# Optimization experiments

Measured on AMD Instinct MI355X. Metric: run time of the kernel, lower is better.

## Reference

```python
import jax, jax.numpy as jnp
import numpy as np

# Sizes: irreps = 16x0e + 8x1o, sh = 1x0e + 1x1o (l_max=1)
N = 50000          # nodes
E = 400000         # edges
MUL0 = 16          # scalar (0e) multiplicity == hidden_dim
MUL1 = 8           # vector (1o) multiplicity
DIM = MUL0 + 3 * MUL1   # 40
RMLP = 64
# FullyConnectedTensorProduct paths (uvw):
#  P1: 0e x 0e -> 0e  w:(16,16)   P2: 1o x 1o -> 0e  w:(8,16)
#  P3: 0e x 1o -> 1o  w:(16,8)    P4: 1o x 0e -> 1o  w:(8,8)
WNUM = MUL0*MUL0 + MUL1*MUL0 + MUL0*MUL1 + MUL1*MUL1  # 576
# e3nn normalization (irrep_normalization='component', path_normalization='element'):
#  out 0e: alpha = 1 / (16*1 + 8*1);  out 1o: alpha = 3 / (16*1 + 8*1)
N0 = float(np.sqrt(1.0 / 24.0))
N1 = float(np.sqrt(3.0 / 24.0))
INV_SQRT3 = float(1.0 / np.sqrt(3.0))  # wigner-3j entries for (1,1,0),(0,1,1),(1,0,1)


def setup_inputs() -> dict:
    key = jax.random.key(0)
    ks = jax.random.split(key, 8)
    h = jax.random.normal(ks[0], (N, DIM), jnp.float32)
    edge_index = jax.random.randint(ks[1], (2, E), 0, N)
    edge_vec = jax.random.normal(ks[2], (E, 3), jnp.float32)
    edge_len = jax.random.uniform(ks[3], (E,), jnp.float32)
    mlp_w1 = jax.random.normal(ks[4], (1, RMLP), jnp.float32)
    mlp_b1 = jnp.zeros((RMLP,), jnp.float32)
    mlp_w2 = jax.random.normal(ks[5], (RMLP, WNUM), jnp.float32) / np.sqrt(RMLP)
    mlp_b2 = jnp.zeros((WNUM,), jnp.float32)
    gate_w = jax.random.normal(ks[6], (MUL0, 3 * MUL1), jnp.float32) / np.sqrt(MUL0)
    gate_b = jnp.zeros((3 * MUL1,), jnp.float32)
    return dict(h=h, edge_index=edge_index, edge_vec=edge_vec, edge_len=edge_len,
                mlp_w1=mlp_w1, mlp_b1=mlp_b1, mlp_w2=mlp_w2, mlp_b2=mlp_b2,
                gate_w=gate_w, gate_b=gate_b)


def reference(h, edge_index, edge_vec, edge_len,
              mlp_w1, mlp_b1, mlp_w2, mlp_b2, gate_w, gate_b):
    sender, receiver = edge_index[0], edge_index[1]
    n = h.shape[0]

    # spherical harmonics, normalize=True, normalization='component'
    # l=0 -> 1.0 ; l=1 -> sqrt(3) * unit(edge_vec)
    unit = edge_vec / jnp.linalg.norm(edge_vec, axis=-1, keepdims=True)
    sh1 = jnp.sqrt(jnp.float32(3.0)) * unit                      # (E,3)

    # radial MLP -> per-edge tensor-product weights
    w = jax.nn.silu(edge_len[:, None] @ mlp_w1 + mlp_b1) @ mlp_w2 + mlp_b2  # (E,576)
    o1 = MUL0 * MUL0; o2 = o1 + MUL1 * MUL0; o3 = o2 + MUL0 * MUL1
    W1 = w[:, :o1].reshape(-1, MUL0, MUL0)
    W2 = w[:, o1:o2].reshape(-1, MUL1, MUL0)
    W3 = w[:, o2:o3].reshape(-1, MUL0, MUL1)
    W4 = w[:, o3:].reshape(-1, MUL1, MUL1)

    # gather sender features and split into scalars / vectors
    hg = h[sender]                                                # (E,40)
    hs = hg[:, :MUL0]                                             # (E,16)
    hv = hg[:, MUL0:].reshape(-1, MUL1, 3)                        # (E,8,3)

    # tensor product (per-edge weighted CG contraction)
    dot = jnp.einsum('euk,ek->eu', hv, sh1)                       # 1o.1o -> 0e
    out_s = N0 * (jnp.einsum('eu,euw->ew', hs, W1)
                  + INV_SQRT3 * jnp.einsum('eu,euw->ew', dot, W2))  # (E,16)
    t3 = jnp.einsum('eu,euw->ew', hs, W3)                         # (E,8)
    t4 = jnp.einsum('euk,euw->ewk', hv, W4)                       # (E,8,3)
    out_v = (N1 * INV_SQRT3) * (t3[:, :, None] * sh1[:, None, :] + t4)

    msg = jnp.concatenate([out_s, out_v.reshape(-1, 3 * MUL1)], axis=-1)  # (E,40)

    # scatter-add into nodes
    agg = jax.ops.segment_sum(msg, receiver, num_segments=n)      # (N,40)

    # scalar gating of non-scalar channels + residual
    gate = jax.nn.sigmoid(h[:, :MUL0] @ gate_w + gate_b)          # (N,24)
    agg = jnp.concatenate([agg[:, :MUL0], agg[:, MUL0:] * gate], axis=-1)
    return h + agg
```

## Files before the change

### kernel.cpp

```cpp
#include <hip/hip_runtime.h>
#include <hip/hip_fp16.h>

typedef _Float16 half8  __attribute__((ext_vector_type(8)));
typedef _Float16 half2v __attribute__((ext_vector_type(2)));
typedef float    float4v __attribute__((ext_vector_type(4)));

namespace {
constexpr int N_NODES = 50000;
constexpr int N_EDGES = 400000;
constexpr int MUL0 = 16;
constexpr int MUL1 = 8;
constexpr int DIM  = 40;
constexpr int RMLP = 64;
constexpr int WNUM = 576;
constexpr int GE   = 256;
constexpr int NGROUP = (N_EDGES + GE - 1) / GE;
constexpr int GRID = 256;
constexpr int WST = 80, AST = 80, FST = 56;
constexpr int OFF_ACT  = 92160;
constexpr int OFF_FEAT = 133120;
constexpr int OFF_RCV  = 161792;
constexpr int LDS_BYTES = 162816;
constexpr float C_N0 = 0.2041241452319315f;
constexpr float C_NV = 0.3535533905932738f * 0.5773502691896258f;
constexpr float C_INV3 = 0.5773502691896258f;
constexpr float C_SQRT3 = 1.7320508075688772f;
}

#define MFMA16(a, b, c) __builtin_amdgcn_mfma_f32_16x16x32_f16((a), (b), (c), 0, 0, 0)

__device__ inline void h2_atomic_add(__half2* addr, __half2 val) {
#if __has_builtin(__builtin_amdgcn_flat_atomic_fadd_v2f16)
    half2v v = *reinterpret_cast<half2v*>(&val);
    (void)__builtin_amdgcn_flat_atomic_fadd_v2f16(
        reinterpret_cast<half2v*>(addr), v);
#else
    unsigned int* ai = reinterpret_cast<unsigned int*>(addr);
    unsigned int old = *ai, assumed;
    do {
        assumed = old;
        __half2 cur = *reinterpret_cast<__half2*>(&assumed);
        __half2 sum = __hadd2(cur, val);
        unsigned int nv = *reinterpret_cast<unsigned int*>(&sum);
        old = atomicCAS(ai, assumed, nv);
    } while (old != assumed);
#endif
}

__global__ __launch_bounds__(512, 1) void edge_fused3(
    const float* __restrict__ h,
    const int*   __restrict__ ei,
    const float* __restrict__ evec,
    const float* __restrict__ elen,
    const float* __restrict__ w1,
    const float* __restrict__ b1,
    const float* __restrict__ w2,
    const float* __restrict__ b2,
    __half2*     __restrict__ agg2)
{
    extern __shared__ char smem[];
    _Float16* w2L  = (_Float16*)smem;
    _Float16* actL = (_Float16*)(smem + OFF_ACT);
    _Float16* featL= (_Float16*)(smem + OFF_FEAT);
    int*      rcvL = (int*)(smem + OFF_RCV);

    const int t = threadIdx.x;

    for (int i = t; i < RMLP * WNUM; i += 512) {
        const int r = i / WNUM;
        const int j = i - r * WNUM;
        w2L[j * WST + r] = (_Float16)w2[i];
    }

    const int lane = t & 63, wid = t >> 6;
    const int l15 = lane & 15, lg = lane >> 4;
    const int usel = lg >> 1;

    __half2 pOS[2][2];
    __half2 pV[2][6];
    int pR[2] = {0, 0};
    int pValid[2] = {0, 0};
    bool havePrev = false;

    for (int g = blockIdx.x; g < NGROUP; g += GRID) {
        if (havePrev) {
#pragma unroll
            for (int tt = 0; tt < 2; ++tt) {
                if (pValid[tt]) {
                    __half2* a2 = agg2 + (long)pR[tt] * 20;
                    h2_atomic_add(a2 + lg * 2 + 0, pOS[tt][0]);
                    h2_atomic_add(a2 + lg * 2 + 1, pOS[tt][1]);
                    if (lg < 2) {
#pragma unroll
                        for (int r2 = 0; r2 < 6; ++r2)
                            h2_atomic_add(a2 + 8 + 6 * lg + r2, pV[tt][r2]);
                    }
                }
            }
        }

        const int base = g * GE;
        const int cnt = (N_EDGES - base < GE) ? (N_EDGES - base) : GE;

        {
            const int el = t >> 1, q = t & 1;
            _Float16* fr = featL + el * FST;
            if (el < cnt) {
                const int eg = base + el;
                const int snd = ei[eg];
                const float* hp = h + (long)snd * DIM;
#pragma unroll
                for (int i = 0; i < 20; ++i)
                    fr[q * 20 + i] = (_Float16)hp[q * 20 + i];
                if (q == 0) {
                    rcvL[el] = ei[N_EDGES + eg];
                    const float v0 = evec[3 * eg + 0];
                    const float v1 = evec[3 * eg + 1];
                    const float v2 = evec[3 * eg + 2];
                    const float rinv = rsqrtf(v0 * v0 + v1 * v1 + v2 * v2) * C_SQRT3;
                    fr[40] = (_Float16)(v0 * rinv);
                    fr[41] = (_Float16)(v1 * rinv);
                    fr[42] = (_Float16)(v2 * rinv);
                }
                const float len = elen[eg];
#pragma unroll
                for (int i = 0; i < 4; ++i) {
                    half8 av;
#pragma unroll
                    for (int j2 = 0; j2 < 8; ++j2) {
                        const int r = q * 32 + i * 8 + j2;
                        const float tv = fmaf(len, w1[r], b1[r]);
                        av[j2] = (_Float16)(tv / (1.0f + __expf(-tv)));
                    }
                    *(half8*)&actL[el * AST + q * 32 + i * 8] = av;
                }
            } else {
                const half8 z = {};
#pragma unroll
                for (int i = 0; i < 20; ++i) fr[q * 20 + i] = (_Float16)0.f;
                if (q == 0) {
                    rcvL[el] = 0;
                    fr[40] = fr[41] = fr[42] = (_Float16)0.f;
                }
#pragma unroll
                for (int i = 0; i < 4; ++i)
                    *(half8*)&actL[el * AST + q * 32 + i * 8] = z;
            }
        }
        __syncthreads();

        {
            const int el = t >> 1;
            const int ub = (t & 1) * 4;
            const _Float16* fr = featL + el * FST;
            const float s0 = (float)fr[40], s1 = (float)fr[41], s2 = (float)fr[42];
#pragma unroll
            for (int j2 = 0; j2 < 4; ++j2) {
                const int u = ub + j2;
                const float d = (float)fr[16 + 3 * u + 0] * s0
                              + (float)fr[16 + 3 * u + 1] * s1
                              + (float)fr[16 + 3 * u + 2] * s2;
                featL[el * FST + 44 + u] = (_Float16)(C_INV3 * d);
            }
        }
        __syncthreads();

        {
            const int et0 = wid * 2;
            half8 B[2][2];
#pragma unroll
            for (int tt = 0; tt < 2; ++tt)
#pragma unroll
                for (int s = 0; s < 2; ++s)
                    B[tt][s] = *(const half8*)&actL[((et0 + tt) * 16 + l15) * AST + s * 32 + lg * 8];

            const float4v zz = {0.f, 0.f, 0.f, 0.f};
            float4v os0 = zz, os1 = zz;
            float4v t30 = zz, t31 = zz;
            float4v t4a0 = zz, t4a1 = zz, t4a2 = zz;
            float4v t4b0 = zz, t4b1 = zz, t4b2 = zz;

            const _Float16* fA = featL + ((et0 + 0) * 16 + l15) * FST;
            const _Float16* fB = featL + ((et0 + 1) * 16 + l15) * FST;

#pragma unroll
            for (int jp = 0; jp < 8; ++jp) {
                const half2v hA = *(const half2v*)&fA[2 * jp];
                const half2v hB = *(const half2v*)&fB[2 * jp];
#pragma unroll
                for (int h2 = 0; h2 < 2; ++h2) {
                    const int jt = 2 * jp + h2;
                    const float4v binit = *(const float4v*)&b2[jt * 16 + lg * 4];
                    const _Float16* wr = &w2L[(jt * 16 + l15) * WST];
                    const half8 w0 = *(const half8*)&wr[lg * 8];
                    const half8 w1v = *(const half8*)&wr[32 + lg * 8];
                    float4v d0 = MFMA16(w0, B[0][0], binit); d0 = MFMA16(w1v, B[0][1], d0);
                    float4v d1 = MFMA16(w0, B[1][0], binit); d1 = MFMA16(w1v, B[1][1], d1);
                    os0 += (float)hA[h2] * d0;
                    os1 += (float)hB[h2] * d1;
                }
            }
#pragma unroll
            for (int jp = 0; jp < 4; ++jp) {
                const half2v hA = *(const half2v*)&fA[44 + 2 * jp];
                const half2v hB = *(const half2v*)&fB[44 + 2 * jp];
#pragma unroll
                for (int h2 = 0; h2 < 2; ++h2) {
                    const int jt = 16 + 2 * jp + h2;
                    const float4v binit = *(const float4v*)&b2[jt * 16 + lg * 4];
                    const _Float16* wr = &w2L[(jt * 16 + l15) * WST];
                    const half8 w0 = *(const half8*)&wr[lg * 8];
                    const half8 w1v = *(const half8*)&wr[32 + lg * 8];
                    float4v d0 = MFMA16(w0, B[0][0], binit); d0 = MFMA16(w1v, B[0][1], d0);
                    float4v d1 = MFMA16(w0, B[1][0], binit); d1 = MFMA16(w1v, B[1][1], d1);
                    os0 += (float)hA[h2] * d0;
                    os1 += (float)hB[h2] * d1;
                }
            }
#pragma unroll
            for (int jt = 24; jt < 32; ++jt) {
                const int u = 2 * (jt - 24) + usel;
                const float4v binit = *(const float4v*)&b2[jt * 16 + lg * 4];
                const _Float16* wr = &w2L[(jt * 16 + l15) * WST];
                const half8 w0 = *(const half8*)&wr[lg * 8];
                const half8 w1v = *(const half8*)&wr[32 + lg * 8];
                float4v d0 = MFMA16(w0, B[0][0], binit); d0 = MFMA16(w1v, B[0][1], d0);
                float4v d1 = MFMA16(w0, B[1][0], binit); d1 = MFMA16(w1v, B[1][1], d1);
                t30 += (float)fA[u] * d0;
                t31 += (float)fB[u] * d1;
            }
#pragma unroll
            for (int jt = 32; jt < 36; ++jt) {
                const int u = 2 * (jt - 32) + usel;
                const float4v binit = *(const float4v*)&b2[jt * 16 + lg * 4];
                const _Float16* wr = &w2L[(jt * 16 + l15) * WST];
                const half8 w0 = *(const half8*)&wr[lg * 8];
                const half8 w1v = *(const half8*)&wr[32 + lg * 8];
                float4v d0 = MFMA16(w0, B[0][0], binit); d0 = MFMA16(w1v, B[0][1], d0);
                float4v d1 = MFMA16(w0, B[1][0], binit); d1 = MFMA16(w1v, B[1][1], d1);
                t4a0 += (float)fA[16 + 3 * u + 0] * d0;
                t4a1 += (float)fA[16 + 3 * u + 1] * d0;
                t4a2 += (float)fA[16 + 3 * u + 2] * d0;
                t4b0 += (float)fB[16 + 3 * u + 0] * d1;
                t4b1 += (float)fB[16 + 3 * u + 1] * d1;
                t4b2 += (float)fB[16 + 3 * u + 2] * d1;
            }

#pragma unroll
            for (int r = 0; r < 4; ++r) {
                t30[r] += __shfl_xor(t30[r], 32);
                t31[r] += __shfl_xor(t31[r], 32);
                t4a0[r] += __shfl_xor(t4a0[r], 32);
                t4a1[r] += __shfl_xor(t4a1[r], 32);
                t4a2[r] += __shfl_xor(t4a2[r], 32);
                t4b0[r] += __shfl_xor(t4b0[r], 32);
                t4b1[r] += __shfl_xor(t4b1[r], 32);
                t4b2[r] += __shfl_xor(t4b2[r], 32);
            }

#pragma unroll
            for (int tt = 0; tt < 2; ++tt) {
                const int el = (et0 + tt) * 16 + l15;
                pValid[tt] = (el < cnt);
                pR[tt] = rcvL[el];
                const float4v& os = tt ? os1 : os0;
                pOS[tt][0] = __floats2half2_rn(C_N0 * os[0], C_N0 * os[1]);
                pOS[tt][1] = __floats2half2_rn(C_N0 * os[2], C_N0 * os[3]);
                const _Float16* fr = featL + el * FST;
                const float s0 = (float)fr[40], s1 = (float)fr[41], s2 = (float)fr[42];
                const float4v& t3 = tt ? t31 : t30;
                const float4v& x0 = tt ? t4b0 : t4a0;
                const float4v& x1 = tt ? t4b1 : t4a1;
                const float4v& x2 = tt ? t4b2 : t4a2;
                float vv[12];
#pragma unroll
                for (int r = 0; r < 4; ++r) {
                    vv[3 * r + 0] = C_NV * (x0[r] + t3[r] * s0);
                    vv[3 * r + 1] = C_NV * (x1[r] + t3[r] * s1);
                    vv[3 * r + 2] = C_NV * (x2[r] + t3[r] * s2);
                }
#pragma unroll
                for (int r2 = 0; r2 < 6; ++r2)
                    pV[tt][r2] = __floats2half2_rn(vv[2 * r2], vv[2 * r2 + 1]);
            }
        }
        __syncthreads();
        havePrev = true;
    }

    if (havePrev) {
#pragma unroll
        for (int tt = 0; tt < 2; ++tt) {
            if (pValid[tt]) {
                __half2* a2 = agg2 + (long)pR[tt] * 20;
                h2_atomic_add(a2 + lg * 2 + 0, pOS[tt][0]);
                h2_atomic_add(a2 + lg * 2 + 1, pOS[tt][1]);
                if (lg < 2) {
#pragma unroll
                    for (int r2 = 0; r2 < 6; ++r2)
                        h2_atomic_add(a2 + 8 + 6 * lg + r2, pV[tt][r2]);
                }
            }
        }
    }
}

__global__ __launch_bounds__(256) void node_kernel2(
    const float* __restrict__ h,
    const float* __restrict__ gw,
    const float* __restrict__ gb,
    const __half2* __restrict__ agg2,
    float*       __restrict__ out)
{
    const int n = blockIdx.x * 256 + threadIdx.x;
    if (n >= N_NODES) return;
    const float* hp = h + (long)n * DIM;
    float* op = out + (long)n * DIM;
    const __half2* ar = agg2 + (long)n * 20;

    float ag[DIM];
#pragma unroll
    for (int i = 0; i < 20; ++i) {
        const float2 f = __half22float2(ar[i]);
        ag[2 * i] = f.x;
        ag[2 * i + 1] = f.y;
    }

    float hsv[MUL0];
#pragma unroll
    for (int u = 0; u < MUL0; ++u) hsv[u] = hp[u];
#pragma unroll
    for (int i = 0; i < MUL0; ++i) op[i] = hsv[i] + ag[i];

#pragma unroll 1
    for (int j = 0; j < 3 * MUL1; ++j) {
        float a = gb[j];
#pragma unroll
        for (int u = 0; u < MUL0; ++u) a = fmaf(hsv[u], gw[u * (3 * MUL1) + j], a);
        const float g = 1.0f / (1.0f + __expf(-a));
        op[MUL0 + j] = fmaf(ag[MUL0 + j], g, hp[MUL0 + j]);
    }
}

extern "C" void kernel_launch(void* const* d_in, const int* in_sizes, int n_in,
                              void* d_out, int out_size, void* d_ws, size_t ws_size,
                              hipStream_t stream)
{
    const float* h    = (const float*)d_in[0];
    const int*   ei   = (const int*)d_in[1];
    const float* evec = (const float*)d_in[2];
    const float* elen = (const float*)d_in[3];
    const float* w1   = (const float*)d_in[4];
    const float* b1   = (const float*)d_in[5];
    const float* w2   = (const float*)d_in[6];
    const float* b2   = (const float*)d_in[7];
    const float* gw   = (const float*)d_in[8];
    const float* gb   = (const float*)d_in[9];
    float* out = (float*)d_out;
    __half2* agg2 = (__half2*)d_ws;

    (void)hipFuncSetAttribute((const void*)edge_fused3,
                              hipFuncAttributeMaxDynamicSharedMemorySize,
                              LDS_BYTES);

    (void)hipMemsetAsync(d_ws, 0, (size_t)N_NODES * DIM * sizeof(__half), stream);
    edge_fused3<<<GRID, 512, LDS_BYTES, stream>>>(
        h, ei, evec, elen, w1, b1, w2, b2, agg2);
    node_kernel2<<<(N_NODES + 255) / 256, 256, 0, stream>>>(h, gw, gb, agg2, out);
}
```

Baseline: 359.2 us.

## Replace atomic scatter with CSR sort and per-node gather of edge messages

Builds a receiver-sorted CSR permutation each call (histogram, single-block scan, fill) and has the edge kernel write per-edge fp16 messages to a buffer, not atomically adding into node accumulators. A new node kernel gathers each node's messages through the permutation, sums them in fp32, and applies gating and the residual. This removes the fp16 packed atomics and the accumulator memset, at the cost of three extra launches, a serial scan over 50k nodes in one block, and writing and re-reading a 32 MB message buffer. The new path runs only if the workspace is large enough; otherwise the old path is kept.

```diff
diff --git a/kernel.cpp b/kernel.cpp
--- a/kernel.cpp
+++ b/kernel.cpp
@@ -2,6 +2,7 @@
 #include <hip/hip_fp16.h>
 
 typedef _Float16 half8  __attribute__((ext_vector_type(8)));
+typedef _Float16 half4s __attribute__((ext_vector_type(4)));
 typedef _Float16 half2v __attribute__((ext_vector_type(2)));
 typedef float    float4v __attribute__((ext_vector_type(4)));
 
@@ -21,6 +22,12 @@
 constexpr int OFF_FEAT = 133120;
 constexpr int OFF_RCV  = 161792;
 constexpr int LDS_BYTES = 162816;
+constexpr size_t MSG_OFF    = 0;
+constexpr size_t PERM_OFF   = 32000000;
+constexpr size_t ROWPTR_OFF = 33600000;
+constexpr size_t CNT_OFF    = 33800064;
+constexpr size_t CUR_OFF    = 34000064;
+constexpr size_t CSR_REQ    = 34200064;
 constexpr float C_N0 = 0.2041241452319315f;
 constexpr float C_NV = 0.3535533905932738f * 0.5773502691896258f;
 constexpr float C_INV3 = 0.5773502691896258f;
@@ -47,6 +54,326 @@
 #endif
 }
 
+__global__ __launch_bounds__(256) void hist_k(const int* __restrict__ ei,
+                                              int* __restrict__ cnt) {
+    const int e = blockIdx.x * 256 + threadIdx.x;
+    if (e < N_EDGES) atomicAdd(&cnt[ei[N_EDGES + e]], 1);
+}
+
+__global__ __launch_bounds__(1024) void scan_k(const int* __restrict__ cnt,
+                                               int* __restrict__ rowptr) {
+    __shared__ int s[1024];
+    const int t = threadIdx.x;
+    constexpr int CH = 49;
+    const int b0 = t * CH;
+    int sum = 0;
+    for (int i = 0; i < CH; ++i) {
+        const int idx = b0 + i;
+        if (idx < N_NODES) sum += cnt[idx];
+    }
+    s[t] = sum;
+    __syncthreads();
+    for (int o = 1; o < 1024; o <<= 1) {
+        const int x = (t >= o) ? s[t - o] : 0;
+        __syncthreads();
+        s[t] += x;
+        __syncthreads();
+    }
+    int run = s[t] - sum;
+    for (int i = 0; i < CH; ++i) {
+        const int idx = b0 + i;
+        if (idx < N_NODES) { rowptr[idx] = run; run += cnt[idx]; }
+    }
+    if (t == 0) rowptr[N_NODES] = N_EDGES;
+}
+
+__global__ __launch_bounds__(256) void fill_k(const int* __restrict__ ei,
+                                              const int* __restrict__ rowptr,
+                                              int* __restrict__ cursor,
+                                              int* __restrict__ perm) {
+    const int e = blockIdx.x * 256 + threadIdx.x;
+    if (e < N_EDGES) {
+        const int r = ei[N_EDGES + e];
+        const int pos = rowptr[r] + atomicAdd(&cursor[r], 1);
+        perm[pos] = e;
+    }
+}
+
+__global__ __launch_bounds__(512, 1) void edge_msg(
+    const float* __restrict__ h,
+    const int*   __restrict__ ei,
+    const float* __restrict__ evec,
+    const float* __restrict__ elen,
+    const float* __restrict__ w1,
+    const float* __restrict__ b1,
+    const float* __restrict__ w2,
+    const float* __restrict__ b2,
+    _Float16*    __restrict__ msg)
+{
+    extern __shared__ char smem[];
+    _Float16* w2L  = (_Float16*)smem;
+    _Float16* actL = (_Float16*)(smem + OFF_ACT);
+    _Float16* featL= (_Float16*)(smem + OFF_FEAT);
+
+    const int t = threadIdx.x;
+    for (int i = t; i < RMLP * WNUM; i += 512) {
+        const int r = i / WNUM;
+        const int j = i - r * WNUM;
+        w2L[j * WST + r] = (_Float16)w2[i];
+    }
+
+    const int lane = t & 63, wid = t >> 6;
+    const int l15 = lane & 15, lg = lane >> 4;
+    const int usel = lg >> 1;
+
+    for (int g = blockIdx.x; g < NGROUP; g += GRID) {
+        const int base = g * GE;
+        const int cntg = (N_EDGES - base < GE) ? (N_EDGES - base) : GE;
+
+        {
+            const int el = t >> 1, q = t & 1;
+            _Float16* fr = featL + el * FST;
+            if (el < cntg) {
+                const int eg = base + el;
+                const int snd = ei[eg];
+                const float4v* hp4 = (const float4v*)(h + (long)snd * DIM);
+#pragma unroll
+                for (int i = 0; i < 5; ++i) {
+                    const float4v v = hp4[q * 5 + i];
+#pragma unroll
+                    for (int k = 0; k < 4; ++k)
+                        fr[q * 20 + 4 * i + k] = (_Float16)v[k];
+                }
+                if (q == 0) {
+                    const float v0 = evec[3 * eg + 0];
+                    const float v1 = evec[3 * eg + 1];
+                    const float v2 = evec[3 * eg + 2];
+                    const float rinv = rsqrtf(v0 * v0 + v1 * v1 + v2 * v2) * C_SQRT3;
+                    fr[40] = (_Float16)(v0 * rinv);
+                    fr[41] = (_Float16)(v1 * rinv);
+                    fr[42] = (_Float16)(v2 * rinv);
+                }
+                const float len = elen[eg];
+#pragma unroll
+                for (int i = 0; i < 4; ++i) {
+                    half8 av;
+#pragma unroll
+                    for (int j2 = 0; j2 < 8; ++j2) {
+                        const int r = q * 32 + i * 8 + j2;
+                        const float tv = fmaf(len, w1[r], b1[r]);
+                        av[j2] = (_Float16)(tv / (1.0f + __expf(-tv)));
+                    }
+                    *(half8*)&actL[el * AST + q * 32 + i * 8] = av;
+                }
+            } else {
+                const half8 z = {};
+#pragma unroll
+                for (int i = 0; i < 20; ++i) fr[q * 20 + i] = (_Float16)0.f;
+                if (q == 0) { fr[40] = fr[41] = fr[42] = (_Float16)0.f; }
+#pragma unroll
+                for (int i = 0; i < 4; ++i)
+                    *(half8*)&actL[el * AST + q * 32 + i * 8] = z;
+            }
+        }
+        __syncthreads();
+
+        {
+            const int el = t >> 1;
+            const int ub = (t & 1) * 4;
+            const _Float16* fr = featL + el * FST;
+            const float s0 = (float)fr[40], s1 = (float)fr[41], s2 = (float)fr[42];
+#pragma unroll
+            for (int j2 = 0; j2 < 4; ++j2) {
+                const int u = ub + j2;
+                const float d = (float)fr[16 + 3 * u + 0] * s0
+                              + (float)fr[16 + 3 * u + 1] * s1
+                              + (float)fr[16 + 3 * u + 2] * s2;
+                featL[el * FST + 44 + u] = (_Float16)(C_INV3 * d);
+            }
+        }
+        __syncthreads();
+
+        {
+            const int et0 = wid * 2;
+            half8 B[2][2];
+#pragma unroll
+            for (int tt = 0; tt < 2; ++tt)
+#pragma unroll
+                for (int s = 0; s < 2; ++s)
+                    B[tt][s] = *(const half8*)&actL[((et0 + tt) * 16 + l15) * AST + s * 32 + lg * 8];
+
+            const float4v zz = {0.f, 0.f, 0.f, 0.f};
+            float4v os0 = zz, os1 = zz;
+            float4v t30 = zz, t31 = zz;
+            float4v t4a0 = zz, t4a1 = zz, t4a2 = zz;
+            float4v t4b0 = zz, t4b1 = zz, t4b2 = zz;
+
+            const _Float16* fA = featL + ((et0 + 0) * 16 + l15) * FST;
+            const _Float16* fB = featL + ((et0 + 1) * 16 + l15) * FST;
+
+#pragma unroll
+            for (int jp = 0; jp < 8; ++jp) {
+                const half2v hA = *(const half2v*)&fA[2 * jp];
+                const half2v hB = *(const half2v*)&fB[2 * jp];
+#pragma unroll
+                for (int h2 = 0; h2 < 2; ++h2) {
+                    const int jt = 2 * jp + h2;
+                    const float4v binit = *(const float4v*)&b2[jt * 16 + lg * 4];
+                    const _Float16* wr = &w2L[(jt * 16 + l15) * WST];
+                    const half8 w0 = *(const half8*)&wr[lg * 8];
+                    const half8 w1v = *(const half8*)&wr[32 + lg * 8];
+                    float4v d0 = MFMA16(w0, B[0][0], binit); d0 = MFMA16(w1v, B[0][1], d0);
+                    float4v d1 = MFMA16(w0, B[1][0], binit); d1 = MFMA16(w1v, B[1][1], d1);
+                    os0 += (float)hA[h2] * d0;
+                    os1 += (float)hB[h2] * d1;
+                }
+            }
+#pragma unroll
+            for (int jp = 0; jp < 4; ++jp) {
+                const half2v hA = *(const half2v*)&fA[44 + 2 * jp];
+                const half2v hB = *(const half2v*)&fB[44 + 2 * jp];
+#pragma unroll
+                for (int h2 = 0; h2 < 2; ++h2) {
+                    const int jt = 16 + 2 * jp + h2;
+                    const float4v binit = *(const float4v*)&b2[jt * 16 + lg * 4];
+                    const _Float16* wr = &w2L[(jt * 16 + l15) * WST];
+                    const half8 w0 = *(const half8*)&wr[lg * 8];
+                    const half8 w1v = *(const half8*)&wr[32 + lg * 8];
+                    float4v d0 = MFMA16(w0, B[0][0], binit); d0 = MFMA16(w1v, B[0][1], d0);
+                    float4v d1 = MFMA16(w0, B[1][0], binit); d1 = MFMA16(w1v, B[1][1], d1);
+                    os0 += (float)hA[h2] * d0;
+                    os1 += (float)hB[h2] * d1;
+                }
+            }
+#pragma unroll
+            for (int jt = 24; jt < 32; ++jt) {
+                const int u = 2 * (jt - 24) + usel;
+                const float4v binit = *(const float4v*)&b2[jt * 16 + lg * 4];
+                const _Float16* wr = &w2L[(jt * 16 + l15) * WST];
+                const half8 w0 = *(const half8*)&wr[lg * 8];
+                const half8 w1v = *(const half8*)&wr[32 + lg * 8];
+                float4v d0 = MFMA16(w0, B[0][0], binit); d0 = MFMA16(w1v, B[0][1], d0);
+                float4v d1 = MFMA16(w0, B[1][0], binit); d1 = MFMA16(w1v, B[1][1], d1);
+                t30 += (float)fA[u] * d0;
+                t31 += (float)fB[u] * d1;
+            }
+#pragma unroll
+            for (int jt = 32; jt < 36; ++jt) {
+                const int u = 2 * (jt - 32) + usel;
+                const float4v binit = *(const float4v*)&b2[jt * 16 + lg * 4];
+                const _Float16* wr = &w2L[(jt * 16 + l15) * WST];
+                const half8 w0 = *(const half8*)&wr[lg * 8];
+                const half8 w1v = *(const half8*)&wr[32 + lg * 8];
+                float4v d0 = MFMA16(w0, B[0][0], binit); d0 = MFMA16(w1v, B[0][1], d0);
+                float4v d1 = MFMA16(w0, B[1][0], binit); d1 = MFMA16(w1v, B[1][1], d1);
+                t4a0 += (float)fA[16 + 3 * u + 0] * d0;
+                t4a1 += (float)fA[16 + 3 * u + 1] * d0;
+                t4a2 += (float)fA[16 + 3 * u + 2] * d0;
+                t4b0 += (float)fB[16 + 3 * u + 0] * d1;
+                t4b1 += (float)fB[16 + 3 * u + 1] * d1;
+                t4b2 += (float)fB[16 + 3 * u + 2] * d1;
+            }
+
+#pragma unroll
+            for (int r = 0; r < 4; ++r) {
+                t30[r] += __shfl_xor(t30[r], 32);
+                t31[r] += __shfl_xor(t31[r], 32);
+                t4a0[r] += __shfl_xor(t4a0[r], 32);
+                t4a1[r] += __shfl_xor(t4a1[r], 32);
+                t4a2[r] += __shfl_xor(t4a2[r], 32);
+                t4b0[r] += __shfl_xor(t4b0[r], 32);
+                t4b1[r] += __shfl_xor(t4b1[r], 32);
+                t4b2[r] += __shfl_xor(t4b2[r], 32);
+            }
+
+#pragma unroll
+            for (int tt = 0; tt < 2; ++tt) {
+                const int el = (et0 + tt) * 16 + l15;
+                if (el < cntg) {
+                    _Float16* mr = msg + (long)(base + el) * DIM;
+                    const float4v& os = tt ? os1 : os0;
+                    half4s o;
+#pragma unroll
+                    for (int r = 0; r < 4; ++r) o[r] = (_Float16)(C_N0 * os[r]);
+                    *(half4s*)&mr[lg * 4] = o;
+                    if (lg < 2) {
+                        const _Float16* fr = featL + el * FST;
+                        const float s0 = (float)fr[40], s1 = (float)fr[41], s2 = (float)fr[42];
+                        const float4v& t3 = tt ? t31 : t30;
+                        const float4v& x0 = tt ? t4b0 : t4a0;
+                        const float4v& x1 = tt ? t4b1 : t4a1;
+                        const float4v& x2 = tt ? t4b2 : t4a2;
+                        float vv[12];
+#pragma unroll
+                        for (int r = 0; r < 4; ++r) {
+                            vv[3 * r + 0] = C_NV * (x0[r] + t3[r] * s0);
+                            vv[3 * r + 1] = C_NV * (x1[r] + t3[r] * s1);
+                            vv[3 * r + 2] = C_NV * (x2[r] + t3[r] * s2);
+                        }
+#pragma unroll
+                        for (int b4 = 0; b4 < 3; ++b4) {
+                            half4s pv;
+#pragma unroll
+                            for (int k = 0; k < 4; ++k) pv[k] = (_Float16)vv[4 * b4 + k];
+                            *(half4s*)&mr[16 + 12 * lg + 4 * b4] = pv;
+                        }
+                    }
+                }
+            }
+        }
+        __syncthreads();
+    }
+}
+
+__global__ __launch_bounds__(256) void node_gather(
+    const float* __restrict__ h,
+    const float* __restrict__ gw,
+    const float* __restrict__ gb,
+    const _Float16* __restrict__ msg,
+    const int*   __restrict__ perm,
+    const int*   __restrict__ rowptr,
+    float*       __restrict__ out)
+{
+    const int t = threadIdx.x;
+    const int n = blockIdx.x * 64 + (t >> 2);
+    const int p = t & 3;
+    if (n >= N_NODES) return;
+    const int beg = rowptr[n], end = rowptr[n + 1];
+
+    float acc[10] = {};
+    for (int i = beg; i < end; ++i) {
+        const int e = perm[i];
+        const _Float16* mr = msg + (long)e * DIM + p * 10;
+#pragma unroll
+        for (int c = 0; c < 5; ++c) {
+            const half2v v = *(const half2v*)&mr[2 * c];
+            acc[2 * c]     += (float)v[0];
+            acc[2 * c + 1] += (float)v[1];
+        }
+    }
+
+    const float* hp = h + (long)n * DIM;
+    float* op = out + (long)n * DIM;
+    float hs[16];
+#pragma unroll
+    for (int u = 0; u < 16; ++u) hs[u] = hp[u];
+
+#pragma unroll
+    for (int k = 0; k < 10; ++k) {
+        const int ch = p * 10 + k;
+        if (ch < MUL0) {
+            op[ch] = hp[ch] + acc[k];
+        } else {
+            const int j = ch - MUL0;
+            float a = gb[j];
+#pragma unroll
+            for (int u = 0; u < 16; ++u) a = fmaf(hs[u], gw[u * 24 + j], a);
+            const float gt = 1.0f / (1.0f + __expf(-a));
+            op[ch] = fmaf(acc[k], gt, hp[ch]);
+        }
+    }
+}
+
 __global__ __launch_bounds__(512, 1) void edge_fused3(
     const float* __restrict__ h,
     const int*   __restrict__ ei,
@@ -65,7 +392,6 @@
     int*      rcvL = (int*)(smem + OFF_RCV);
 
     const int t = threadIdx.x;
-
     for (int i = t; i < RMLP * WNUM; i += 512) {
         const int r = i / WNUM;
         const int j = i - r * WNUM;
@@ -101,7 +427,6 @@
 
         const int base = g * GE;
         const int cnt = (N_EDGES - base < GE) ? (N_EDGES - base) : GE;
-
         {
             const int el = t >> 1, q = t & 1;
             _Float16* fr = featL + el * FST;
@@ -148,7 +473,6 @@
             }
         }
         __syncthreads();
-
         {
             const int el = t >> 1;
             const int ub = (t & 1) * 4;
@@ -164,7 +488,6 @@
             }
         }
         __syncthreads();
-
         {
             const int et0 = wid * 2;
             half8 B[2][2];
@@ -245,7 +568,6 @@
                 t4b1 += (float)fB[16 + 3 * u + 1] * d1;
                 t4b2 += (float)fB[16 + 3 * u + 2] * d1;
             }
-
 #pragma unroll
             for (int r = 0; r < 4; ++r) {
                 t30[r] += __shfl_xor(t30[r], 32);
@@ -257,7 +579,6 @@
                 t4b1[r] += __shfl_xor(t4b1[r], 32);
                 t4b2[r] += __shfl_xor(t4b2[r], 32);
             }
-
 #pragma unroll
             for (int tt = 0; tt < 2; ++tt) {
                 const int el = (et0 + tt) * 16 + l15;
@@ -325,13 +646,11 @@
         ag[2 * i] = f.x;
         ag[2 * i + 1] = f.y;
     }
-
     float hsv[MUL0];
 #pragma unroll
     for (int u = 0; u < MUL0; ++u) hsv[u] = hp[u];
 #pragma unroll
     for (int i = 0; i < MUL0; ++i) op[i] = hsv[i] + ag[i];
-
 #pragma unroll 1
     for (int j = 0; j < 3 * MUL1; ++j) {
         float a = gb[j];
@@ -357,14 +676,33 @@
     const float* gw   = (const float*)d_in[8];
     const float* gb   = (const float*)d_in[9];
     float* out = (float*)d_out;
-    __half2* agg2 = (__half2*)d_ws;
-
+    char* ws = (char*)d_ws;
+
+    (void)hipFuncSetAttribute((const void*)edge_msg,
+                              hipFuncAttributeMaxDynamicSharedMemorySize, LDS_BYTES);
     (void)hipFuncSetAttribute((const void*)edge_fused3,
-                              hipFuncAttributeMaxDynamicSharedMemorySize,
-                              LDS_BYTES);
-
-    (void)hipMemsetAsync(d_ws, 0, (size_t)N_NODES * DIM * sizeof(__half), stream);
-    edge_fused3<<<GRID, 512, LDS_BYTES, stream>>>(
-        h, ei, evec, elen, w1, b1, w2, b2, agg2);
-    node_kernel2<<<(N_NODES + 255) / 256, 256, 0, stream>>>(h, gw, gb, agg2, out);
-}
+                              hipFuncAttributeMaxDynamicSharedMemorySize, LDS_BYTES);
+
+    if (ws_size >= CSR_REQ) {
+        _Float16* msg  = (_Float16*)(ws + MSG_OFF);
+        int* perm      = (int*)(ws + PERM_OFF);
+        int* rowptr    = (int*)(ws + ROWPTR_OFF);
+        int* cnt       = (int*)(ws + CNT_OFF);
+        int* cursor    = (int*)(ws + CUR_OFF);
+
+        (void)hipMemsetAsync(ws + CNT_OFF, 0, 400000, stream);
+        hist_k<<<(N_EDGES + 255) / 256, 256, 0, stream>>>(ei, cnt);
+        scan_k<<<1, 1024, 0, stream>>>(cnt, rowptr);
+        fill_k<<<(N_EDGES + 255) / 256, 256, 0, stream>>>(ei, rowptr, cursor, perm);
+        edge_msg<<<GRID, 512, LDS_BYTES, stream>>>(
+            h, ei, evec, elen, w1, b1, w2, b2, msg);
+        node_gather<<<(N_NODES + 63) / 64, 256, 0, stream>>>(
+            h, gw, gb, msg, perm, rowptr, out);
+    } else {
+        __half2* agg2 = (__half2*)d_ws;
+        (void)hipMemsetAsync(d_ws, 0, (size_t)N_NODES * DIM * sizeof(__half), stream);
+        edge_fused3<<<GRID, 512, LDS_BYTES, stream>>>(
+            h, ei, evec, elen, w1, b1, w2, b2, agg2);
+        node_kernel2<<<(N_NODES + 255) / 256, 256, 0, stream>>>(h, gw, gb, agg2, out);
+    }
+}
```

New measurement: 492.8 us. 37.2% more time.
